# Optimization experiments

Hardware: AMD Instinct MI355X
Metric: run time of the kernel (lower is better)

The kernel has to match this reference:

```python
import jax, jax.numpy as jnp
import numpy as np

B, N, T, H = 32, 16, 64, 256


def setup_inputs() -> dict:
    key = jax.random.key(0)
    k1, k2, k3 = jax.random.split(key, 3)
    node_rnn_output = jax.random.normal(k1, (B, T, H), dtype=jnp.float32)
    neigh_rnn_output = jax.random.normal(k2, (B, N, T, H), dtype=jnp.float32)
    # neighbor counts in [1, N] to avoid divide-by-zero in 1/sqrt scaling
    neighbors_number = jax.random.randint(k3, (B,), 1, N + 1, dtype=jnp.int64)
    return {
        "node_rnn_output": node_rnn_output,
        "neigh_rnn_output": neigh_rnn_output,
        "neighbors_number": neighbors_number,
    }


def reference(node_rnn_output, neigh_rnn_output, neighbors_number):
    b, t, h = node_rnn_output.shape
    n = neigh_rnn_output.shape[1]
    # [B, N*T, H]
    flat_neigh = neigh_rnn_output.reshape(b, n * t, h)
    # repeat node output along time axis: [B, N*T, H]
    stacked_node = jnp.tile(node_rnn_output, (1, n, 1))
    # S = flat_neigh @ stacked_node^T : [B, N*T, N*T]
    S = jnp.einsum("bqh,bkh->bqk", flat_neigh, stacked_node)
    scale = jnp.sqrt(neighbors_number.astype(S.dtype))  # [B]
    S = S / scale[:, None, None]
    A = jax.nn.softmax(S, axis=-1)
    # dropout with p=0 (eval / reference) is identity
    W = A.sum(axis=1).reshape(b, n, t)  # [B, N, T]
    output = jnp.einsum("bqk,bkh->bqh", A, flat_neigh)  # [B, N*T, H]
    return (output, W)
```

## Files before the change

kernel.cpp:

```cpp
#include <hip/hip_runtime.h>

#define Bc  32
#define Nc  16
#define Tc  64
#define Hc  256
#define NTc 1024

typedef unsigned short u16;
using v8s = __attribute__((ext_vector_type(8))) short;
using v4f = __attribute__((ext_vector_type(4))) float;

static __device__ __forceinline__ u16 f2bf(float x) {
    unsigned u = __float_as_uint(x);
    unsigned r = u + 0x7fffu + ((u >> 16) & 1u);
    return (u16)(r >> 16);
}
static __device__ __forceinline__ float bf2f(u16 h) {
    return __uint_as_float(((unsigned)h) << 16);
}

__global__ __launch_bounds__(256) void prep_kernel(const float* __restrict__ neigh,
                                                   u16* __restrict__ MT) {
    __shared__ float Ls[32][68];
    int bk = blockIdx.x, tid = threadIdx.x;

    int b  = bk >> 3;
    int sub = bk & 7;
    int h0 = (sub & 3) << 6;
    int t0 = (sub >> 2) << 5;
#pragma unroll
    for (int rep = 0; rep < 2; rep++) {
        int idx = rep * 256 + tid;
        int t = idx >> 4, c4 = idx & 15;
        const float4* p = (const float4*)(neigh + ((size_t)b * Nc * Tc + t0 + t) * Hc + h0) + c4;
        float4 a = make_float4(0.f, 0.f, 0.f, 0.f);
#pragma unroll
        for (int i = 0; i < Nc; i++) {
            float4 v = p[(size_t)i * (Tc * Hc / 4)];
            a.x += v.x; a.y += v.y; a.z += v.z; a.w += v.w;
        }
        const float r = 1.0f / 16.0f;
        Ls[t][c4 * 4 + 0] = a.x * r;
        Ls[t][c4 * 4 + 1] = a.y * r;
        Ls[t][c4 * 4 + 2] = a.z * r;
        Ls[t][c4 * 4 + 3] = a.w * r;
    }
    __syncthreads();
#pragma unroll
    for (int rep = 0; rep < 2; rep++) {
        int idx = rep * 256 + tid;
        int h = idx >> 3, t4 = idx & 7;
        ushort4 o;
        o.x = f2bf(Ls[t4 * 4 + 0][h]);
        o.y = f2bf(Ls[t4 * 4 + 1][h]);
        o.z = f2bf(Ls[t4 * 4 + 2][h]);
        o.w = f2bf(Ls[t4 * 4 + 3][h]);
        *(ushort4*)(MT + ((size_t)b * Hc + h0 + h) * Tc + t0 + t4 * 4) = o;
    }
}

__global__ __launch_bounds__(256, 2) void fused_kernel(const float* __restrict__ neigh,
                                                       const float* __restrict__ node,
                                                       const int* __restrict__ nbr,
                                                       const u16* __restrict__ MT,
                                                       float* __restrict__ out,
                                                       float* __restrict__ Wpart) {
    __shared__ u16 Xh[64][72];
    __shared__ u16 Xl[64][72];
    __shared__ u16 Nh[64][72];
    __shared__ u16 Nl[64][72];
    __shared__ u16 Ph[64][72];
    __shared__ float Wtmp[256];

    int b  = blockIdx.x >> 4;
    int i  = blockIdx.x & 15;
    int q0 = i << 6;

    int tid  = threadIdx.x;
    int w    = tid >> 6;
    int lane = tid & 63;
    int quad = lane >> 4;
    int c    = lane & 15;

    int nb = (nbr[1] == 0) ? nbr[2 * b] : nbr[b];
    float rscale = rsqrtf((float)nb);

    const float* Xg  = neigh + ((size_t)b * Nc * Tc + q0) * Hc;
    const float* Ng  = node + (size_t)b * Tc * Hc;
    const u16*   MTg = MT + (size_t)b * Hc * Tc;

    v4f acc[4];
#pragma unroll
    for (int nt = 0; nt < 4; nt++)
#pragma unroll
        for (int rg = 0; rg < 4; rg++) acc[nt][rg] = 0.f;

    for (int k0 = 0; k0 < Hc; k0 += 64) {
#pragma unroll
        for (int rep = 0; rep < 4; rep++) {
            int idx = rep * 256 + tid;
            int row = idx >> 4, c4 = idx & 15;
            float4 xv = *(const float4*)(Xg + (size_t)row * Hc + k0 + c4 * 4);
            ushort4 hs, ls;
            hs.x = f2bf(xv.x); ls.x = f2bf(xv.x - bf2f(hs.x));
            hs.y = f2bf(xv.y); ls.y = f2bf(xv.y - bf2f(hs.y));
            hs.z = f2bf(xv.z); ls.z = f2bf(xv.z - bf2f(hs.z));
            hs.w = f2bf(xv.w); ls.w = f2bf(xv.w - bf2f(hs.w));
            *(ushort4*)&Xh[row][c4 * 4] = hs;
            *(ushort4*)&Xl[row][c4 * 4] = ls;
        }
#pragma unroll
        for (int rep = 0; rep < 4; rep++) {
            int idx = rep * 256 + tid;
            int row = idx >> 4, c4 = idx & 15;
            float4 nv = *(const float4*)(Ng + (size_t)row * Hc + k0 + c4 * 4);
            ushort4 hs, ls;
            hs.x = f2bf(nv.x); ls.x = f2bf(nv.x - bf2f(hs.x));
            hs.y = f2bf(nv.y); ls.y = f2bf(nv.y - bf2f(hs.y));
            hs.z = f2bf(nv.z); ls.z = f2bf(nv.z - bf2f(hs.z));
            hs.w = f2bf(nv.w); ls.w = f2bf(nv.w - bf2f(hs.w));
            *(ushort4*)&Nh[row][c4 * 4] = hs;
            *(ushort4*)&Nl[row][c4 * 4] = ls;
        }
        __syncthreads();

#pragma unroll
        for (int ks = 0; ks < 64; ks += 32) {
            v8s ah = *(const v8s*)&Xh[w * 16 + c][ks + quad * 8];
            v8s al = *(const v8s*)&Xl[w * 16 + c][ks + quad * 8];
#pragma unroll
            for (int nt = 0; nt < 4; nt++) {
                v8s bh = *(const v8s*)&Nh[nt * 16 + c][ks + quad * 8];
                v8s bl = *(const v8s*)&Nl[nt * 16 + c][ks + quad * 8];
                acc[nt] = __builtin_amdgcn_mfma_f32_16x16x32_bf16(ah, bh, acc[nt], 0, 0, 0);
                acc[nt] = __builtin_amdgcn_mfma_f32_16x16x32_bf16(ah, bl, acc[nt], 0, 0, 0);
                acc[nt] = __builtin_amdgcn_mfma_f32_16x16x32_bf16(al, bh, acc[nt], 0, 0, 0);
            }
        }
        __syncthreads();
    }

#pragma unroll
    for (int nt = 0; nt < 4; nt++)
#pragma unroll
        for (int rg = 0; rg < 4; rg++) acc[nt][rg] *= rscale;

#pragma unroll
    for (int rg = 0; rg < 4; rg++) {
        float m = fmaxf(fmaxf(acc[0][rg], acc[1][rg]), fmaxf(acc[2][rg], acc[3][rg]));
#pragma unroll
        for (int d = 1; d < 16; d <<= 1) m = fmaxf(m, __shfl_xor(m, d));
        float e0 = __expf(acc[0][rg] - m);
        float e1 = __expf(acc[1][rg] - m);
        float e2 = __expf(acc[2][rg] - m);
        float e3 = __expf(acc[3][rg] - m);
        float s = e0 + e1 + e2 + e3;
#pragma unroll
        for (int d = 1; d < 16; d <<= 1) s += __shfl_xor(s, d);
        float inv = 1.0f / s;
        acc[0][rg] = e0 * inv; acc[1][rg] = e1 * inv;
        acc[2][rg] = e2 * inv; acc[3][rg] = e3 * inv;
    }

#pragma unroll
    for (int nt = 0; nt < 4; nt++) {
        float cs = acc[nt][0] + acc[nt][1] + acc[nt][2] + acc[nt][3];
        cs += __shfl_xor(cs, 16);
        cs += __shfl_xor(cs, 32);
        if (quad == 0) Wtmp[w * 64 + nt * 16 + c] = cs;
    }

#pragma unroll
    for (int nt = 0; nt < 4; nt++)
#pragma unroll
        for (int rg = 0; rg < 4; rg++)
            Ph[w * 16 + quad * 4 + rg][nt * 16 + c] = f2bf(acc[nt][rg]);

    __syncthreads();

    if (tid < 64) {
        float s = Wtmp[tid] + Wtmp[64 + tid] + Wtmp[128 + tid] + Wtmp[192 + tid];
        Wpart[((size_t)b * Nc + i) * Tc + tid] = s;
    }

    v8s pa0 = *(const v8s*)&Ph[w * 16 + c][quad * 8];
    v8s pa1 = *(const v8s*)&Ph[w * 16 + c][32 + quad * 8];

    for (int h0 = 0; h0 < Hc; h0 += 64) {
#pragma unroll
        for (int rep = 0; rep < 2; rep++) {
            int idx = rep * 256 + tid;
            int row = idx >> 3, c8 = idx & 7;
            *(uint4*)&Xh[row][c8 * 8] = *(const uint4*)(MTg + (size_t)(h0 + row) * Tc + c8 * 8);
        }
        __syncthreads();

        v4f oc[4];
#pragma unroll
        for (int ht = 0; ht < 4; ht++)
#pragma unroll
            for (int rg = 0; rg < 4; rg++) oc[ht][rg] = 0.f;

#pragma unroll
        for (int ht = 0; ht < 4; ht++) {
            v8s b0 = *(const v8s*)&Xh[ht * 16 + c][quad * 8];
            v8s b1 = *(const v8s*)&Xh[ht * 16 + c][32 + quad * 8];
            oc[ht] = __builtin_amdgcn_mfma_f32_16x16x32_bf16(pa0, b0, oc[ht], 0, 0, 0);
            oc[ht] = __builtin_amdgcn_mfma_f32_16x16x32_bf16(pa1, b1, oc[ht], 0, 0, 0);
        }

        float* ob = out + ((size_t)b * NTc + q0 + w * 16 + quad * 4) * Hc + h0 + c;
#pragma unroll
        for (int ht = 0; ht < 4; ht++)
#pragma unroll
            for (int rg = 0; rg < 4; rg++)
                ob[(size_t)rg * Hc + ht * 16] = oc[ht][rg];

        __syncthreads();
    }
}

__global__ __launch_bounds__(256) void wexp_kernel(const float* __restrict__ Wpart,
                                                   float* __restrict__ Wout) {
    int idx = blockIdx.x * 256 + threadIdx.x;
    int b = idx >> 10;
    int t = idx & 63;
    const float* wp = Wpart + (size_t)b * Nc * Tc + t;
    float s = 0.f;
#pragma unroll
    for (int ip = 0; ip < Nc; ip++) s += wp[ip * Tc];
    Wout[idx] = s * (1.0f / 16.0f);
}

extern "C" void kernel_launch(void* const* d_in, const int* in_sizes, int n_in,
                              void* d_out, int out_size, void* d_ws, size_t ws_size,
                              hipStream_t stream) {
    const float* node  = (const float*)d_in[0];
    const float* neigh = (const float*)d_in[1];
    const int*   nbr   = (const int*)d_in[2];

    float* out = (float*)d_out;

    u16*   MTw   = (u16*)d_ws;
    float* Wpart = (float*)(MTw + (size_t)Bc * Hc * Tc);

    prep_kernel <<<256, 256, 0, stream>>>(neigh, MTw);
    fused_kernel<<<512, 256, 0, stream>>>(neigh, node, nbr, MTw, out, Wpart);
    wexp_kernel <<<128, 256, 0, stream>>>(Wpart, out + (size_t)Bc * NTc * Hc);
}
```

Measured before the change: 105.4 us.

## Fuse neighbor-mean prep into main kernel with per-batch atomic counter sync

Removes the separate prep kernel. Each block of the fused kernel now computes four time rows of the bf16 neighbor-mean transpose and publishes them with relaxed atomic stores, then bumps a per-batch counter. Before the output GEMM, each block spin-waits until all 16 blocks of its batch have contributed. The block index is also remapped so that one batch's 16 blocks land on the same XCD, improving L2 locality. The cost is a memset launch plus an inter-block spin wait, which relies on all blocks of a batch being co-resident and carries a deadlock risk that is only softened by the guard counter.

```diff
diff --git a/kernel.cpp b/kernel.cpp
--- a/kernel.cpp
+++ b/kernel.cpp
@@ -19,62 +19,27 @@
     return __uint_as_float(((unsigned)h) << 16);
 }
 
-__global__ __launch_bounds__(256) void prep_kernel(const float* __restrict__ neigh,
-                                                   u16* __restrict__ MT) {
-    __shared__ float Ls[32][68];
-    int bk = blockIdx.x, tid = threadIdx.x;
-
-    int b  = bk >> 3;
-    int sub = bk & 7;
-    int h0 = (sub & 3) << 6;
-    int t0 = (sub >> 2) << 5;
-#pragma unroll
-    for (int rep = 0; rep < 2; rep++) {
-        int idx = rep * 256 + tid;
-        int t = idx >> 4, c4 = idx & 15;
-        const float4* p = (const float4*)(neigh + ((size_t)b * Nc * Tc + t0 + t) * Hc + h0) + c4;
-        float4 a = make_float4(0.f, 0.f, 0.f, 0.f);
-#pragma unroll
-        for (int i = 0; i < Nc; i++) {
-            float4 v = p[(size_t)i * (Tc * Hc / 4)];
-            a.x += v.x; a.y += v.y; a.z += v.z; a.w += v.w;
-        }
-        const float r = 1.0f / 16.0f;
-        Ls[t][c4 * 4 + 0] = a.x * r;
-        Ls[t][c4 * 4 + 1] = a.y * r;
-        Ls[t][c4 * 4 + 2] = a.z * r;
-        Ls[t][c4 * 4 + 3] = a.w * r;
-    }
-    __syncthreads();
-#pragma unroll
-    for (int rep = 0; rep < 2; rep++) {
-        int idx = rep * 256 + tid;
-        int h = idx >> 3, t4 = idx & 7;
-        ushort4 o;
-        o.x = f2bf(Ls[t4 * 4 + 0][h]);
-        o.y = f2bf(Ls[t4 * 4 + 1][h]);
-        o.z = f2bf(Ls[t4 * 4 + 2][h]);
-        o.w = f2bf(Ls[t4 * 4 + 3][h]);
-        *(ushort4*)(MT + ((size_t)b * Hc + h0 + h) * Tc + t0 + t4 * 4) = o;
-    }
-}
-
 __global__ __launch_bounds__(256, 2) void fused_kernel(const float* __restrict__ neigh,
                                                        const float* __restrict__ node,
                                                        const int* __restrict__ nbr,
-                                                       const u16* __restrict__ MT,
+                                                       u16* __restrict__ MT,
                                                        float* __restrict__ out,
-                                                       float* __restrict__ Wpart) {
+                                                       float* __restrict__ Wpart,
+                                                       int* __restrict__ cnt) {
     __shared__ u16 Xh[64][72];
     __shared__ u16 Xl[64][72];
     __shared__ u16 Nh[64][72];
     __shared__ u16 Nl[64][72];
     __shared__ u16 Ph[64][72];
     __shared__ float Wtmp[256];
-
-    int b  = blockIdx.x >> 4;
-    int i  = blockIdx.x & 15;
-    int q0 = i << 6;
+    __shared__ float Msc[4][264];
+
+    int raw  = blockIdx.x;
+    int xcd  = raw & 7;
+    int slot = raw >> 3;
+    int b    = (xcd << 2) + (slot >> 4);
+    int i    = slot & 15;
+    int q0   = i << 6;
 
     int tid  = threadIdx.x;
     int w    = tid >> 6;
@@ -85,9 +50,42 @@
     int nb = (nbr[1] == 0) ? nbr[2 * b] : nbr[b];
     float rscale = rsqrtf((float)nb);
 
-    const float* Xg  = neigh + ((size_t)b * Nc * Tc + q0) * Hc;
+    const float* neighb = neigh + (size_t)b * Nc * Tc * Hc;
+    const float* Xg  = neighb + (size_t)q0 * Hc;
     const float* Ng  = node + (size_t)b * Tc * Hc;
-    const u16*   MTg = MT + (size_t)b * Hc * Tc;
+    u16*         MTb = MT + (size_t)b * Hc * Tc;
+
+    {
+        int tr = 4 * i + w;
+        const float* rp = neighb + (size_t)tr * Hc + lane * 4;
+        float4 a = make_float4(0.f, 0.f, 0.f, 0.f);
+#pragma unroll
+        for (int ip = 0; ip < Nc; ip++) {
+            float4 v = *(const float4*)(rp + (size_t)ip * Tc * Hc);
+            a.x += v.x; a.y += v.y; a.z += v.z; a.w += v.w;
+        }
+        const float r = 1.0f / 16.0f;
+        Msc[w][lane * 4 + 0] = a.x * r;
+        Msc[w][lane * 4 + 1] = a.y * r;
+        Msc[w][lane * 4 + 2] = a.z * r;
+        Msc[w][lane * 4 + 3] = a.w * r;
+    }
+    __syncthreads();
+    {
+        int h = tid;
+        unsigned long long val =
+            (unsigned long long)f2bf(Msc[0][h]) |
+            ((unsigned long long)f2bf(Msc[1][h]) << 16) |
+            ((unsigned long long)f2bf(Msc[2][h]) << 32) |
+            ((unsigned long long)f2bf(Msc[3][h]) << 48);
+        __hip_atomic_store((unsigned long long*)(MTb + (size_t)h * Tc + 4 * i),
+                           val, __ATOMIC_RELAXED, __HIP_MEMORY_SCOPE_AGENT);
+    }
+    __syncthreads();
+    if (tid == 0) {
+        __threadfence();
+        __hip_atomic_fetch_add(&cnt[b], 1, __ATOMIC_RELEASE, __HIP_MEMORY_SCOPE_AGENT);
+    }
 
     v4f acc[4];
 #pragma unroll
@@ -183,6 +181,14 @@
         Wpart[((size_t)b * Nc + i) * Tc + tid] = s;
     }
 
+    if (tid == 0) {
+        int guard = 1 << 21;
+        while (__hip_atomic_load(&cnt[b], __ATOMIC_ACQUIRE, __HIP_MEMORY_SCOPE_AGENT) < 16
+               && --guard)
+            __builtin_amdgcn_s_sleep(8);
+    }
+    __syncthreads();
+
     v8s pa0 = *(const v8s*)&Ph[w * 16 + c][quad * 8];
     v8s pa1 = *(const v8s*)&Ph[w * 16 + c][32 + quad * 8];
 
@@ -191,7 +197,7 @@
         for (int rep = 0; rep < 2; rep++) {
             int idx = rep * 256 + tid;
             int row = idx >> 3, c8 = idx & 7;
-            *(uint4*)&Xh[row][c8 * 8] = *(const uint4*)(MTg + (size_t)(h0 + row) * Tc + c8 * 8);
+            *(uint4*)&Xh[row][c8 * 8] = *(const uint4*)(MTb + (size_t)(h0 + row) * Tc + c8 * 8);
         }
         __syncthreads();
 
@@ -243,8 +249,9 @@
 
     u16*   MTw   = (u16*)d_ws;
     float* Wpart = (float*)(MTw + (size_t)Bc * Hc * Tc);
-
-    prep_kernel <<<256, 256, 0, stream>>>(neigh, MTw);
-    fused_kernel<<<512, 256, 0, stream>>>(neigh, node, nbr, MTw, out, Wpart);
+    int*   cnt   = (int*)(Wpart + (size_t)Bc * Nc * Tc);
+
+    hipMemsetAsync(cnt, 0, Bc * sizeof(int), stream);
+    fused_kernel<<<512, 256, 0, stream>>>(neigh, node, nbr, MTw, out, Wpart, cnt);
     wexp_kernel <<<128, 256, 0, stream>>>(Wpart, out + (size_t)Bc * NTc * Hc);
 }
```

Result: slower. 127.0 us (+20.6%).
